# Kernel tuning notes

Hardware: AMD Instinct MI355X
Metric: run time of the kernel (lower is better)

## Reference

```python
import jax, jax.numpy as jnp
import numpy as np

N = 100000      # nodes per graph
E = 1600000     # edges (avg degree 16)
T = 4           # time steps
NL = 15         # num_locations
FD = 3          # feature_dim_node
H, C = 2, 6     # heads, per-head channels (hidden_channels=12)
HC = H * C


def setup_inputs():
    key = jax.random.key(0)
    ks = jax.random.split(key, 24)
    inp = {
        'node_types': jax.random.randint(ks[0], (T, N), 0, 4, dtype=jnp.int32),
        'requests': jax.random.normal(ks[1], (T, N), jnp.float32),
        'time_index': jax.random.uniform(ks[2], (T, N), dtype=jnp.float32),
        'edge_index': jax.random.randint(ks[3], (T, 2, E), 0, N, dtype=jnp.int32),
        'emb': 0.1 * jax.random.normal(ks[4], (4, FD), jnp.float32),
    }
    dims = [FD + 2, HC, HC, HC]
    k = 5
    for i, din in enumerate(dims):
        inp[f'W{i}'] = jax.random.normal(ks[k], (din, HC), jnp.float32) / np.sqrt(din); k += 1
        inp[f'as{i}'] = 0.1 * jax.random.normal(ks[k], (H, C), jnp.float32); k += 1
        inp[f'ad{i}'] = 0.1 * jax.random.normal(ks[k], (H, C), jnp.float32); k += 1
        inp[f'b{i}'] = jnp.zeros((HC,), jnp.float32); k += 1
    return inp


def gat_layer(x, src, dst, W, a_s, a_d, b):
    # PyG GATConv: linear -> per-head additive attention -> softmax over incoming
    # edges (self-loops already appended to src/dst) -> weighted aggregation.
    h = (x @ W).reshape(N, H, C)
    e_s = (h * a_s).sum(-1)                                  # [N, H]
    e_d = (h * a_d).sum(-1)                                  # [N, H]
    logits = jax.nn.leaky_relu(e_s[src] + e_d[dst], 0.2)      # [E', H]
    m = jax.ops.segment_max(logits, dst, num_segments=N)
    m = jnp.where(jnp.isfinite(m), m, 0.0)
    p = jnp.exp(logits - m[dst])
    denom = jax.ops.segment_sum(p, dst, num_segments=N)
    alpha = p / (denom[dst] + 1e-16)
    out = jax.ops.segment_sum(alpha[:, :, None] * h[src], dst, num_segments=N)
    return out.reshape(N, HC) + b


def _forward(node_types, requests, time_index, edge_index, emb, params):
    def step(nt, req, ti, ei):
        x_emb = emb[nt]                                       # [N, FD]
        tail = req[NL:]
        mean = tail.mean()
        std = tail.std(ddof=1)                                # torch.std is unbiased
        req_f = jnp.concatenate([req[:NL], (tail - mean) / std])
        x = jnp.concatenate([x_emb, req_f[:, None], ti[:, None]], axis=-1)  # [N, FD+2]
        loops = jnp.arange(N, dtype=ei.dtype)
        src = jnp.concatenate([ei[0], loops])
        dst = jnp.concatenate([ei[1], loops])
        for i in range(3):                                     # att + 2 hidden_atts
            x = jax.nn.relu(gat_layer(x, src, dst, *params[i]))
        return gat_layer(x, src, dst, *params[3])              # final_att, no act
    return jax.vmap(step)(node_types, requests, time_index, edge_index)


def reference(node_types, requests, time_index, edge_index, emb,
              W0, as0, ad0, b0, W1, as1, ad1, b1,
              W2, as2, ad2, b2, W3, as3, ad3, b3):
    params = [(W0, as0, ad0, b0), (W1, as1, ad1, b1),
              (W2, as2, ad2, b2), (W3, as3, ad3, b3)]
    return _forward(node_types, requests, time_index, edge_index, emb, params)
```

## Files before the change

### kernel.cpp

```cpp
#include <hip/hip_runtime.h>
#include <hip/hip_fp16.h>
#include <math.h>

#define NN 100000
#define EE 1600000
#define TT 4
#define NLQ 15
#define FDQ 3
#define HCQ 12
#define CAP 48
#define RECU 8
#define NCB64 ((NN + 63) / 64)
#define BKT 512
#define NBKT ((NN + BKT - 1) / BKT)
#define EB 4096
#define NBE ((EE + EB - 1) / EB)
#define SPB 64

typedef int v4i __attribute__((ext_vector_type(4)));

__device__ __forceinline__ unsigned pack2(float a, float b) {
    __half2 h = __floats2half2_rn(a, b);
    return *reinterpret_cast<unsigned*>(&h);
}
__device__ __forceinline__ float2 unpack2(unsigned u) {
    __half2 h = *reinterpret_cast<__half2*>(&u);
    return __half22float2(h);
}

__global__ void statsA(const float* __restrict__ req, float* __restrict__ part) {
    int t = blockIdx.y, b = blockIdx.x;
    const float* r = req + (size_t)t * NN;
    const int NP = NN - NLQ;
    __shared__ float ssum[256], ssq[256];
    float s = 0.f, q = 0.f;
    for (int i = b * 256 + threadIdx.x; i < NP; i += SPB * 256) {
        float v = r[NLQ + i]; s += v; q += v * v;
    }
    ssum[threadIdx.x] = s; ssq[threadIdx.x] = q;
    __syncthreads();
    for (int off = 128; off > 0; off >>= 1) {
        if ((int)threadIdx.x < off) {
            ssum[threadIdx.x] += ssum[threadIdx.x + off];
            ssq[threadIdx.x]  += ssq[threadIdx.x + off];
        }
        __syncthreads();
    }
    if (threadIdx.x == 0) {
        part[(t * SPB + b) * 2]     = ssum[0];
        part[(t * SPB + b) * 2 + 1] = ssq[0];
    }
}

__global__ void statsB(const float* __restrict__ part, float* __restrict__ stats) {
    int t = blockIdx.x, k = threadIdx.x;
    __shared__ float ssum[64], ssq[64];
    ssum[k] = part[(t * SPB + k) * 2];
    ssq[k]  = part[(t * SPB + k) * 2 + 1];
    __syncthreads();
    for (int off = 32; off > 0; off >>= 1) {
        if (k < off) { ssum[k] += ssum[k + off]; ssq[k] += ssq[k + off]; }
        __syncthreads();
    }
    if (k == 0) {
        float n = (float)(NN - NLQ);
        float mean = ssum[0] / n;
        float var  = (ssq[0] - ssum[0] * mean) / (n - 1.0f);
        stats[t * 2]     = mean;
        stats[t * 2 + 1] = 1.0f / sqrtf(var);
    }
}

__global__ void histE(const int* __restrict__ ei, int* __restrict__ bh) {
    int t = blockIdx.y, b = blockIdx.x;
    __shared__ int h[NBKT];
    for (int i = threadIdx.x; i < NBKT; i += 256) h[i] = 0;
    __syncthreads();
    int base = b * EB;
    for (int k = 0; k < EB; k += 256) {
        int e = base + k + threadIdx.x;
        if (e < EE) {
            int dst = __builtin_nontemporal_load(ei + (size_t)t * 2 * EE + EE + e);
            atomicAdd(&h[dst >> 9], 1);
        }
    }
    __syncthreads();
    for (int i = threadIdx.x; i < NBKT; i += 256)
        bh[((size_t)t * NBE + b) * NBKT + i] = h[i];
}

__global__ void scanT(const int* __restrict__ bh, int* __restrict__ bhoff, int* __restrict__ tot) {
    int k = blockIdx.x, t = blockIdx.y;
    __shared__ int sv[512];
    int b = threadIdx.x;
    int v = (b < NBE) ? bh[((size_t)t * NBE + b) * NBKT + k] : 0;
    sv[b] = v;
    __syncthreads();
    for (int off = 1; off < 512; off <<= 1) {
        int x = (b >= off) ? sv[b - off] : 0;
        __syncthreads();
        sv[b] += x;
        __syncthreads();
    }
    if (b < NBE) bhoff[((size_t)t * NBE + b) * NBKT + k] = sv[b] - v;
    if (b == NBE - 1) tot[t * NBKT + k] = sv[b];
}

__global__ void baseT(const int* __restrict__ tot, int* __restrict__ bbase) {
    int t = blockIdx.x, k = threadIdx.x;
    __shared__ int sv[256];
    int v = (k < NBKT) ? tot[t * NBKT + k] : 0;
    sv[k] = v;
    __syncthreads();
    for (int off = 1; off < 256; off <<= 1) {
        int x = (k >= off) ? sv[k - off] : 0;
        __syncthreads();
        sv[k] += x;
        __syncthreads();
    }
    if (k < NBKT) bbase[t * (NBKT + 1) + k] = sv[k] - v;
    if (k == NBKT - 1) bbase[t * (NBKT + 1) + NBKT] = sv[k];
}

__global__ void scatE2(const int* __restrict__ ei, const int* __restrict__ bh,
                       const int* __restrict__ bhoff, const int* __restrict__ bbase,
                       unsigned* __restrict__ bke) {
    int t = blockIdx.y, b = blockIdx.x;
    __shared__ unsigned sorted[EB];
    __shared__ unsigned char bid[EB];
    __shared__ int loff[NBKT], cur[NBKT], goff[NBKT];
    __shared__ int sv[256];
    int k = threadIdx.x;
    int v = (k < NBKT) ? bh[((size_t)t * NBE + b) * NBKT + k] : 0;
    sv[k] = v;
    __syncthreads();
    for (int off = 1; off < 256; off <<= 1) {
        int x = (k >= off) ? sv[k - off] : 0;
        __syncthreads();
        sv[k] += x;
        __syncthreads();
    }
    if (k < NBKT) {
        int ex = sv[k] - v;
        loff[k] = ex;
        cur[k]  = ex;
        goff[k] = bbase[t * (NBKT + 1) + k]
                + bhoff[((size_t)t * NBE + b) * NBKT + k] - ex;
    }
    __syncthreads();
    int base = b * EB;
    int nvalid = (EE - base < EB) ? (EE - base) : EB;
    for (int e = threadIdx.x; e < nvalid; e += 256) {
        int src = __builtin_nontemporal_load(ei + (size_t)t * 2 * EE + base + e);
        int dst = __builtin_nontemporal_load(ei + (size_t)t * 2 * EE + EE + base + e);
        int bk = dst >> 9;
        int lp = atomicAdd(&cur[bk], 1);
        sorted[lp] = ((unsigned)(dst & 511) << 17) | (unsigned)src;
        bid[lp] = (unsigned char)bk;
    }
    __syncthreads();
    for (int p = threadIdx.x; p < nvalid; p += 256) {
        int B = bid[p];
        bke[(size_t)t * EE + goff[B] + p] = sorted[p];
    }
}

__global__ void fillv2(const unsigned* __restrict__ bke, const int* __restrict__ bbase,
                       int* __restrict__ cnt, int* __restrict__ csr) {
    extern __shared__ int sm[];
    int* cl    = sm;
    int* slots = sm + BKT;
    int t = blockIdx.y, b = blockIdx.x;
    int nbase = b * BKT;
    int nn = (NN - nbase < BKT) ? (NN - nbase) : BKT;
    for (int i = threadIdx.x; i < nn; i += 256) {
        cl[i] = 1;
        slots[i * CAP] = nbase + i;
    }
    __syncthreads();
    int beg = bbase[t * (NBKT + 1) + b], end = bbase[t * (NBKT + 1) + b + 1];
    const unsigned* bkt_ = bke + (size_t)t * EE;
    int nE = end - beg;
    for (int base0 = 0; base0 < nE; base0 += 1024) {
        unsigned pk[4];
#pragma unroll
        for (int j = 0; j < 4; j++) {
            int e = beg + base0 + j * 256 + threadIdx.x;
            pk[j] = (e < end) ? bkt_[e] : 0xFFFFFFFFu;
        }
#pragma unroll
        for (int j = 0; j < 4; j++) {
            if (pk[j] != 0xFFFFFFFFu) {
                int dl = pk[j] >> 17, src = (int)(pk[j] & 0x1FFFF);
                int pos = atomicAdd(&cl[dl], 1);
                slots[dl * CAP + pos] = src;
            }
        }
    }
    __syncthreads();
    const v4i* sl4 = (const v4i*)slots;
    v4i* dst4 = (v4i*)(csr + ((size_t)t * NN + nbase) * CAP);
    int tot4 = nn * CAP / 4;
    for (int i = threadIdx.x; i < tot4; i += 256)
        __builtin_nontemporal_store(sl4[i], dst4 + i);
    for (int i = threadIdx.x; i < nn; i += 256)
        cnt[t * NN + nbase + i] = cl[i];
}

__global__ void node0_kernel(const int* __restrict__ nt, const float* __restrict__ req,
                             const float* __restrict__ ti, const float* __restrict__ emb,
                             const float* __restrict__ W, const float* __restrict__ as_,
                             const float* __restrict__ ad_, const float* __restrict__ stats,
                             unsigned* __restrict__ hrec, float* __restrict__ ed) {
    __shared__ float sW[5 * HCQ], sas[HCQ], sad[HCQ];
    if (threadIdx.x < 5 * HCQ) sW[threadIdx.x] = W[threadIdx.x];
    if (threadIdx.x < HCQ) { sas[threadIdx.x] = as_[threadIdx.x]; sad[threadIdx.x] = ad_[threadIdx.x]; }
    __syncthreads();
    int id = blockIdx.x * blockDim.x + threadIdx.x;
    if (id >= TT * NN) return;
    int t = id / NN, n = id - t * NN;
    float mean = stats[t * 2], rstd = stats[t * 2 + 1];
    int typ = nt[id];
    float x[5];
    x[0] = emb[typ * FDQ + 0];
    x[1] = emb[typ * FDQ + 1];
    x[2] = emb[typ * FDQ + 2];
    float rv = req[id];
    x[3] = (n < NLQ) ? rv : (rv - mean) * rstd;
    x[4] = ti[id];
    float hv[HCQ];
#pragma unroll
    for (int c = 0; c < HCQ; c++) {
        float a = 0.f;
#pragma unroll
        for (int k = 0; k < 5; k++) a += x[k] * sW[k * HCQ + c];
        hv[c] = a;
    }
    float e0 = 0.f, e1 = 0.f, f0 = 0.f, f1 = 0.f;
#pragma unroll
    for (int c = 0; c < 6; c++) {
        e0 += hv[c] * sas[c];     f0 += hv[c] * sad[c];
        e1 += hv[6 + c] * sas[6 + c]; f1 += hv[6 + c] * sad[6 + c];
    }
    uint4* rp = (uint4*)(hrec + (size_t)id * RECU);
    rp[0] = make_uint4(pack2(hv[0], hv[1]), pack2(hv[2], hv[3]), pack2(hv[4], hv[5]), pack2(hv[6], hv[7]));
    rp[1] = make_uint4(pack2(hv[8], hv[9]), pack2(hv[10], hv[11]), __float_as_uint(e0), __float_as_uint(e1));
    ((float2*)ed)[id] = make_float2(f0, f1);
}

__global__ void edge_kernel(const int* __restrict__ cnt, const int* __restrict__ csr_src,
                            const unsigned* __restrict__ hrecI, const float* __restrict__ edI,
                            const float* __restrict__ bias,
                            const float* __restrict__ Wn, const float* __restrict__ asn,
                            const float* __restrict__ adn,
                            unsigned* __restrict__ hrecO, float* __restrict__ edO,
                            float* __restrict__ outF, int mode) {
    __shared__ float sb[HCQ], sW[HCQ * HCQ], sas[HCQ], sad[HCQ];
    if (threadIdx.x < HCQ) sb[threadIdx.x] = bias[threadIdx.x];
    if (mode == 0) {
        if (threadIdx.x < HCQ * HCQ) sW[threadIdx.x] = Wn[threadIdx.x];
        if (threadIdx.x < HCQ) { sas[threadIdx.x] = asn[threadIdx.x]; sad[threadIdx.x] = adn[threadIdx.x]; }
    }
    __syncthreads();
    int b = blockIdx.x;
    int t = b & 3;
    int nl = threadIdx.x >> 2, q = threadIdx.x & 3;
    int n = (b >> 2) * 64 + nl;
    if (n >= NN) return;
    int id = t * NN + n;
    int deg = cnt[id];
    const int*      srcs = csr_src + (size_t)id * CAP;
    const unsigned* hb   = hrecI + (size_t)t * NN * RECU;
    float2 edv = ((const float2*)edI)[id];
    float ed0 = edv.x, ed1 = edv.y;
    float d0 = 0.f, d1 = 0.f;
    float acc[HCQ];
#pragma unroll
    for (int c = 0; c < HCQ; c++) acc[c] = 0.f;

    auto process = [&](int4 s4, int ebase) {
        int rem = deg - ebase;
        int ss[4];
        ss[0] = s4.x;
        ss[1] = (rem > 1) ? s4.y : 0;
        ss[2] = (rem > 2) ? s4.z : 0;
        ss[3] = (rem > 3) ? s4.w : 0;
        uint4 ra[4], rb[4];
#pragma unroll
        for (int k = 0; k < 4; k++) {
            const uint4* hp = (const uint4*)(hb + (size_t)ss[k] * RECU);
            ra[k] = hp[0];
            rb[k] = hp[1];
        }
#pragma unroll
        for (int k = 0; k < 4; k++) {
            float valid = (rem > k) ? 1.0f : 0.0f;
            float l0 = __uint_as_float(rb[k].z) + ed0; l0 = fmaxf(l0, 0.2f * l0);
            float l1 = __uint_as_float(rb[k].w) + ed1; l1 = fmaxf(l1, 0.2f * l1);
            float w0 = __expf(l0) * valid, w1 = __expf(l1) * valid;
            d0 += w0; d1 += w1;
            float2 h01 = unpack2(ra[k].x), h23 = unpack2(ra[k].y), h45 = unpack2(ra[k].z);
            float2 h67 = unpack2(ra[k].w), h89 = unpack2(rb[k].x), hab = unpack2(rb[k].y);
            acc[0] += w0 * h01.x;  acc[1] += w0 * h01.y;
            acc[2] += w0 * h23.x;  acc[3] += w0 * h23.y;
            acc[4] += w0 * h45.x;  acc[5] += w0 * h45.y;
            acc[6] += w1 * h67.x;  acc[7] += w1 * h67.y;
            acc[8]  += w1 * h89.x; acc[9]  += w1 * h89.y;
            acc[10] += w1 * hab.x; acc[11] += w1 * hab.y;
        }
    };

    int e0 = q * 4;
    int4 sA = *(const int4*)(srcs + e0);
    int4 sB = *(const int4*)(srcs + 16 + e0);
    if (e0 < deg) process(sA, e0);
    if (16 + e0 < deg) {
        process(sB, 16 + e0);
        if (32 + e0 < deg) {
            int4 sC = *(const int4*)(srcs + 32 + e0);
            process(sC, 32 + e0);
        }
    }

#pragma unroll
    for (int m = 1; m <= 2; m <<= 1) {
        d0 += __shfl_xor(d0, m);
        d1 += __shfl_xor(d1, m);
#pragma unroll
        for (int c = 0; c < HCQ; c++) acc[c] += __shfl_xor(acc[c], m);
    }
    if (q != 0) return;

    float inv0 = 1.0f / (d0 + 1e-16f);
    float inv1 = 1.0f / (d1 + 1e-16f);
    float ov[HCQ];
#pragma unroll
    for (int c = 0; c < HCQ; c++)
        ov[c] = acc[c] * ((c < 6) ? inv0 : inv1) + sb[c];

    if (mode == 1) {
        float4* op = (float4*)(outF + (size_t)id * HCQ);
        op[0] = make_float4(ov[0], ov[1], ov[2], ov[3]);
        op[1] = make_float4(ov[4], ov[5], ov[6], ov[7]);
        op[2] = make_float4(ov[8], ov[9], ov[10], ov[11]);
        return;
    }
#pragma unroll
    for (int c = 0; c < HCQ; c++) ov[c] = fmaxf(ov[c], 0.f);
    float hv[HCQ];
#pragma unroll
    for (int c = 0; c < HCQ; c++) {
        float a = 0.f;
#pragma unroll
        for (int k = 0; k < HCQ; k++) a += ov[k] * sW[k * HCQ + c];
        hv[c] = a;
    }
    float e0f = 0.f, e1f = 0.f, f0 = 0.f, f1 = 0.f;
#pragma unroll
    for (int c = 0; c < 6; c++) {
        e0f += hv[c] * sas[c];     f0 += hv[c] * sad[c];
        e1f += hv[6 + c] * sas[6 + c]; f1 += hv[6 + c] * sad[6 + c];
    }
    uint4* rp = (uint4*)(hrecO + (size_t)id * RECU);
    rp[0] = make_uint4(pack2(hv[0], hv[1]), pack2(hv[2], hv[3]), pack2(hv[4], hv[5]), pack2(hv[6], hv[7]));
    rp[1] = make_uint4(pack2(hv[8], hv[9]), pack2(hv[10], hv[11]), __float_as_uint(e0f), __float_as_uint(e1f));
    ((float2*)edO)[id] = make_float2(f0, f1);
}

extern "C" void kernel_launch(void* const* d_in, const int* in_sizes, int n_in,
                              void* d_out, int out_size, void* d_ws, size_t ws_size,
                              hipStream_t stream) {
    const int*   nt  = (const int*)d_in[0];
    const float* req = (const float*)d_in[1];
    const float* ti  = (const float*)d_in[2];
    const int*   ei  = (const int*)d_in[3];
    const float* emb = (const float*)d_in[4];
    const float* W[4], *as_[4], *ad_[4], *bb[4];
    for (int l = 0; l < 4; l++) {
        W[l]   = (const float*)d_in[5 + l * 4 + 0];
        as_[l] = (const float*)d_in[5 + l * 4 + 1];
        ad_[l] = (const float*)d_in[5 + l * 4 + 2];
        bb[l]  = (const float*)d_in[5 + l * 4 + 3];
    }

    char* p = (char*)d_ws;
    auto alloc = [&](size_t bytes) -> void* {
        void* r = (void*)p;
        p += (bytes + 255) & ~(size_t)255;
        return r;
    };
    float*    stats = (float*)alloc((size_t)TT * 2 * 4);
    float*    part  = (float*)alloc((size_t)TT * SPB * 2 * 4);
    int*      cnt   = (int*)  alloc((size_t)TT * NN * 4);
    unsigned* hrecA = (unsigned*)alloc((size_t)TT * NN * RECU * 4);
    float*    edA   = (float*)alloc((size_t)TT * NN * 2 * 4);
    int*      bh    = (int*)  alloc((size_t)TT * NBE * NBKT * 4);
    int*      bhoff = (int*)  alloc((size_t)TT * NBE * NBKT * 4);
    int*      tot   = (int*)  alloc((size_t)TT * NBKT * 4);
    int*      bbase = (int*)  alloc((size_t)TT * (NBKT + 1) * 4);
    char*     ub    = (char*)alloc((size_t)TT * EE * 4);
    unsigned* bke   = (unsigned*)ub;
    unsigned* hrecB = (unsigned*)ub;
    float*    edB   = (float*)(ub + (size_t)TT * NN * RECU * 4);
    int*      csr   = (int*)  alloc((size_t)TT * NN * CAP * 4);

    statsA<<<dim3(SPB, TT), 256, 0, stream>>>(req, part);
    statsB<<<TT, 64, 0, stream>>>(part, stats);

    histE<<<dim3(NBE, TT), 256, 0, stream>>>(ei, bh);
    scanT<<<dim3(NBKT, TT), 512, 0, stream>>>(bh, bhoff, tot);
    baseT<<<TT, 256, 0, stream>>>(tot, bbase);
    scatE2<<<dim3(NBE, TT), 256, 0, stream>>>(ei, bh, bhoff, bbase, bke);
    size_t fillLds = (size_t)(BKT + BKT * CAP) * 4;
    fillv2<<<dim3(NBKT, TT), 256, fillLds, stream>>>(bke, bbase, cnt, csr);

    int ngrid = (TT * NN + 255) / 256;
    int egrid2 = 4 * NCB64;
    node0_kernel<<<ngrid, 256, 0, stream>>>(nt, req, ti, emb, W[0], as_[0], ad_[0], stats, hrecA, edA);
    edge_kernel<<<egrid2, 256, 0, stream>>>(cnt, csr, hrecA, edA, bb[0], W[1], as_[1], ad_[1],
                                            hrecB, edB, nullptr, 0);
    edge_kernel<<<egrid2, 256, 0, stream>>>(cnt, csr, hrecB, edB, bb[1], W[2], as_[2], ad_[2],
                                            hrecA, edA, nullptr, 0);
    edge_kernel<<<egrid2, 256, 0, stream>>>(cnt, csr, hrecA, edA, bb[2], W[3], as_[3], ad_[3],
                                            hrecB, edB, nullptr, 0);
    edge_kernel<<<egrid2, 256, 0, stream>>>(cnt, csr, hrecB, edB, bb[3], nullptr, nullptr, nullptr,
                                            nullptr, nullptr, (float*)d_out, 1);
}
```

Before: 455.9 us.

## Use eight lanes per node in GAT edge kernel and split epilogue transform

```diff
diff --git a/kernel.cpp b/kernel.cpp
--- a/kernel.cpp
+++ b/kernel.cpp
@@ -10,7 +10,7 @@
 #define HCQ 12
 #define CAP 48
 #define RECU 8
-#define NCB64 ((NN + 63) / 64)
+#define NCB32 ((NN + 31) / 32)
 #define BKT 512
 #define NBKT ((NN + BKT - 1) / BKT)
 #define EB 4096
@@ -264,8 +264,8 @@
     __syncthreads();
     int b = blockIdx.x;
     int t = b & 3;
-    int nl = threadIdx.x >> 2, q = threadIdx.x & 3;
-    int n = (b >> 2) * 64 + nl;
+    int nl = threadIdx.x >> 3, q = threadIdx.x & 7;
+    int n = (b >> 2) * 32 + nl;
     if (n >= NN) return;
     int id = t * NN + n;
     int deg = cnt[id];
@@ -310,26 +310,24 @@
         }
     };
 
-    int e0 = q * 4;
-    int4 sA = *(const int4*)(srcs + e0);
-    int4 sB = *(const int4*)(srcs + 16 + e0);
-    if (e0 < deg) process(sA, e0);
-    if (16 + e0 < deg) {
-        process(sB, 16 + e0);
-        if (32 + e0 < deg) {
-            int4 sC = *(const int4*)(srcs + 32 + e0);
-            process(sC, 32 + e0);
-        }
-    }
-
-#pragma unroll
-    for (int m = 1; m <= 2; m <<= 1) {
+    int e0s = q * 4;
+    int4 sA = *(const int4*)(srcs + e0s);
+    if (e0s < deg) process(sA, e0s);
+    if (q < 4) {
+        int e2 = 32 + q * 4;
+        if (e2 < deg) {
+            int4 sC = *(const int4*)(srcs + e2);
+            process(sC, e2);
+        }
+    }
+
+#pragma unroll
+    for (int m = 1; m <= 4; m <<= 1) {
         d0 += __shfl_xor(d0, m);
         d1 += __shfl_xor(d1, m);
 #pragma unroll
         for (int c = 0; c < HCQ; c++) acc[c] += __shfl_xor(acc[c], m);
     }
-    if (q != 0) return;
 
     float inv0 = 1.0f / (d0 + 1e-16f);
     float inv1 = 1.0f / (d1 + 1e-16f);
@@ -339,32 +337,43 @@
         ov[c] = acc[c] * ((c < 6) ? inv0 : inv1) + sb[c];
 
     if (mode == 1) {
-        float4* op = (float4*)(outF + (size_t)id * HCQ);
-        op[0] = make_float4(ov[0], ov[1], ov[2], ov[3]);
-        op[1] = make_float4(ov[4], ov[5], ov[6], ov[7]);
-        op[2] = make_float4(ov[8], ov[9], ov[10], ov[11]);
+        if (q == 0) {
+            float4* op = (float4*)(outF + (size_t)id * HCQ);
+            op[0] = make_float4(ov[0], ov[1], ov[2], ov[3]);
+            op[1] = make_float4(ov[4], ov[5], ov[6], ov[7]);
+            op[2] = make_float4(ov[8], ov[9], ov[10], ov[11]);
+        }
         return;
     }
+    if (q >= 2) return;
 #pragma unroll
     for (int c = 0; c < HCQ; c++) ov[c] = fmaxf(ov[c], 0.f);
-    float hv[HCQ];
-#pragma unroll
-    for (int c = 0; c < HCQ; c++) {
+    int base = q * 6;
+    float hv[6];
+#pragma unroll
+    for (int j = 0; j < 6; j++) {
         float a = 0.f;
 #pragma unroll
-        for (int k = 0; k < HCQ; k++) a += ov[k] * sW[k * HCQ + c];
-        hv[c] = a;
-    }
-    float e0f = 0.f, e1f = 0.f, f0 = 0.f, f1 = 0.f;
-#pragma unroll
-    for (int c = 0; c < 6; c++) {
-        e0f += hv[c] * sas[c];     f0 += hv[c] * sad[c];
-        e1f += hv[6 + c] * sas[6 + c]; f1 += hv[6 + c] * sad[6 + c];
-    }
+        for (int k = 0; k < HCQ; k++) a += ov[k] * sW[k * HCQ + base + j];
+        hv[j] = a;
+    }
+    float ee = 0.f, ff = 0.f;
+#pragma unroll
+    for (int j = 0; j < 6; j++) { ee += hv[j] * sas[base + j]; ff += hv[j] * sad[base + j]; }
+    unsigned w0 = pack2(hv[0], hv[1]);
+    unsigned w1 = pack2(hv[2], hv[3]);
+    unsigned w2 = pack2(hv[4], hv[5]);
+    unsigned eeu = __float_as_uint(ee);
+    unsigned send = (q == 0) ? eeu : w0;
+    unsigned recv = __shfl_xor(send, 1);
+    float fo = __shfl_xor(ff, 1);
     uint4* rp = (uint4*)(hrecO + (size_t)id * RECU);
-    rp[0] = make_uint4(pack2(hv[0], hv[1]), pack2(hv[2], hv[3]), pack2(hv[4], hv[5]), pack2(hv[6], hv[7]));
-    rp[1] = make_uint4(pack2(hv[8], hv[9]), pack2(hv[10], hv[11]), __float_as_uint(e0f), __float_as_uint(e1f));
-    ((float2*)edO)[id] = make_float2(f0, f1);
+    if (q == 0) {
+        rp[0] = make_uint4(w0, w1, w2, recv);
+        ((float2*)edO)[id] = make_float2(ff, fo);
+    } else {
+        rp[1] = make_uint4(w1, w2, recv, eeu);
+    }
 }
 
 extern "C" void kernel_launch(void* const* d_in, const int* in_sizes, int n_in,
@@ -415,7 +424,7 @@
     fillv2<<<dim3(NBKT, TT), 256, fillLds, stream>>>(bke, bbase, cnt, csr);
 
     int ngrid = (TT * NN + 255) / 256;
-    int egrid2 = 4 * NCB64;
+    int egrid2 = 4 * NCB32;
     node0_kernel<<<ngrid, 256, 0, stream>>>(nt, req, ti, emb, W[0], as_[0], ad_[0], stats, hrecA, edA);
     edge_kernel<<<egrid2, 256, 0, stream>>>(cnt, csr, hrecA, edA, bb[0], W[1], as_[1], ad_[1],
                                             hrecB, edB, nullptr, 0);
```

Result: no change. 453.6 us (-0.5%).
